# Optimization experiments

Measured on AMD Instinct MI355X. Metric: run time of the kernel, lower is better.

The kernel has to match this reference:

```python
import jax, jax.numpy as jnp
import numpy as np

H = 256          # hidden_dim
NH = 4           # num_heads
HD = H // NH     # head_dim = 64
EPS = 1e-5


def _ln(x, g, b):
    m = jnp.mean(x, axis=-1, keepdims=True)
    v = jnp.mean(jnp.square(x - m), axis=-1, keepdims=True)
    return (x - m) * jax.lax.rsqrt(v + EPS) * g + b


def _mha1(q_in, kv_in, in_proj_w, in_proj_b, out_w, out_b):
    # Single-query / single-key multihead attention (seq_len == 1 on both sides).
    # q_in, kv_in: [B, H]
    Wq, Wk, Wv = jnp.split(in_proj_w, 3, axis=0)   # each [H, H]
    bq, bk, bv = jnp.split(in_proj_b, 3, axis=0)
    B = q_in.shape[0]
    q = (q_in @ Wq.T + bq).reshape(B, NH, HD)
    k = (kv_in @ Wk.T + bk).reshape(B, NH, HD)
    v = (kv_in @ Wv.T + bv).reshape(B, NH, HD)
    scores = jnp.sum(q * k, axis=-1, keepdims=True) / jnp.sqrt(jnp.float32(HD))  # [B,NH,1]
    w = jax.nn.softmax(scores, axis=-1)  # softmax over 1 key -> all ones
    out = (w * v).reshape(B, H)
    return out @ out_w.T + out_b


def setup_inputs() -> dict:
    key = jax.random.key(0)
    ks = jax.random.split(key, 16)
    B, BIO, TXT, NC = 65536, 32, 768, 2
    s = lambda n: 1.0 / np.sqrt(n)
    return {
        "bio": jax.random.normal(ks[0], (B, BIO), jnp.float32),
        "text": jax.random.normal(ks[1], (B, TXT), jnp.float32),
        "bio_w": jax.random.normal(ks[2], (H, BIO), jnp.float32) * s(BIO),
        "bio_b": jnp.zeros((H,), jnp.float32),
        "text_w": jax.random.normal(ks[3], (H, TXT), jnp.float32) * s(TXT),
        "text_b": jnp.zeros((H,), jnp.float32),
        "ln_bio_g": jnp.ones((H,), jnp.float32),
        "ln_bio_b": jnp.zeros((H,), jnp.float32),
        "ln_text_g": jnp.ones((H,), jnp.float32),
        "ln_text_b": jnp.zeros((H,), jnp.float32),
        "in_proj_w": jax.random.normal(ks[4], (3 * H, H), jnp.float32) * s(H),
        "in_proj_b": jnp.zeros((3 * H,), jnp.float32),
        "out_w": jax.random.normal(ks[5], (H, H), jnp.float32) * s(H),
        "out_b": jnp.zeros((H,), jnp.float32),
        "cls1_w": jax.random.normal(ks[6], (H, 2 * H), jnp.float32) * s(2 * H),
        "cls1_b": jnp.zeros((H,), jnp.float32),
        "cls_ln_g": jnp.ones((H,), jnp.float32),
        "cls_ln_b": jnp.zeros((H,), jnp.float32),
        "cls2_w": jax.random.normal(ks[7], (NC, H), jnp.float32) * s(H),
        "cls2_b": jnp.zeros((NC,), jnp.float32),
    }


def reference(bio, text, bio_w, bio_b, text_w, text_b, ln_bio_g, ln_bio_b,
              ln_text_g, ln_text_b, in_proj_w, in_proj_b, out_w, out_b,
              cls1_w, cls1_b, cls_ln_g, cls_ln_b, cls2_w, cls2_b):
    b = _ln(bio @ bio_w.T + bio_b, ln_bio_g, ln_bio_b)      # [B, H]
    t = _ln(text @ text_w.T + text_b, ln_text_g, ln_text_b)  # [B, H]
    attn_bio = _mha1(b, t, in_proj_w, in_proj_b, out_w, out_b)
    attn_text = _mha1(t, b, in_proj_w, in_proj_b, out_w, out_b)
    fused = jnp.concatenate([attn_bio, attn_text], axis=-1)  # [B, 2H]
    h = jax.nn.relu(_ln(fused @ cls1_w.T + cls1_b, cls_ln_g, cls_ln_b))
    return h @ cls2_w.T + cls2_b
```

## Files before the change

### kernel.cpp

```cpp
#include <hip/hip_runtime.h>

typedef __attribute__((ext_vector_type(4))) float f4;
typedef __attribute__((ext_vector_type(2))) float f2;
typedef __attribute__((ext_vector_type(8))) short s8;

#define EPS 1e-5f

__device__ __forceinline__ unsigned short f2bf(float f) {
    union { float f; unsigned u; } v; v.f = f;
    unsigned u = v.u;
    return (unsigned short)((u + 0x7fffu + ((u >> 16) & 1u)) >> 16);
}
__device__ __forceinline__ unsigned pack2(float a, float b) {
    return (unsigned)f2bf(a) | ((unsigned)f2bf(b) << 16);
}

__device__ __forceinline__ unsigned cvt_pk2(float a, float b) {
    unsigned r;
    asm("v_cvt_pk_bf16_f32 %0, %1, %2" : "=v"(r) : "v"(a), "v"(b));
    return r;
}
__device__ __forceinline__ unsigned short cvt1(float a) {
    return (unsigned short)cvt_pk2(a, a);
}
__device__ __forceinline__ s8 pack8(f4 a, f4 b) {
    union { s8 v; unsigned u[4]; } r;
    r.u[0] = cvt_pk2(a[0], a[1]); r.u[1] = cvt_pk2(a[2], a[3]);
    r.u[2] = cvt_pk2(b[0], b[1]); r.u[3] = cvt_pk2(b[2], b[3]);
    return r.v;
}

#if defined(__has_builtin)
#if __has_builtin(__builtin_amdgcn_global_load_lds)
#define HAVE_GLLDS 1
#endif
#endif
__device__ __forceinline__ void gl_lds16(const float* g, unsigned short* l) {
#ifdef HAVE_GLLDS
    __builtin_amdgcn_global_load_lds(
        (const __attribute__((address_space(1))) unsigned int*)g,
        (__attribute__((address_space(3))) unsigned int*)l, 16, 0, 0);
#else
    *(f4*)l = *(const f4*)g;
#endif
}

__global__ __launch_bounds__(256) void k_prep1(const float* __restrict__ text_w,
                                               const float* __restrict__ bio_w,
                                               const float* __restrict__ out_w,
                                               const float* __restrict__ in_proj_w,
                                               const float* __restrict__ in_proj_b,
                                               const float* __restrict__ out_b,
                                               unsigned short* __restrict__ twFL,
                                               unsigned short* __restrict__ bwFL,
                                               float* __restrict__ A,
                                               float* __restrict__ cvec) {
    int b = blockIdx.x, t = threadIdx.x;
    if (b < 96) {
        int idx = b * 256 + t;
        int ksg = idx >> 10;
        int rem = idx & 1023;
        int ct = rem >> 6, lane = rem & 63;
        int n  = ct * 16 + (lane & 15);
        int k0 = ksg * 32 + ((lane >> 4) << 3);
        const float* src = &text_w[n * 768 + k0];
        f4 a = *(const f4*)src, c = *(const f4*)(src + 4);
        unsigned* dst = (unsigned*)&twFL[idx * 8];
        dst[0] = pack2(a[0], a[1]); dst[1] = pack2(a[2], a[3]);
        dst[2] = pack2(c[0], c[1]); dst[3] = pack2(c[2], c[3]);
    } else if (b < 100) {
        int idx = (b - 96) * 256 + t;
        int ct = idx >> 6, lane = idx & 63;
        int n  = ct * 16 + (lane & 15);
        int k0 = (lane >> 4) << 3;
        const float* src = &bio_w[n * 32 + k0];
        f4 a = *(const f4*)src, c = *(const f4*)(src + 4);
        unsigned* dst = (unsigned*)&bwFL[idx * 8];
        dst[0] = pack2(a[0], a[1]); dst[1] = pack2(a[2], a[3]);
        dst[2] = pack2(c[0], c[1]); dst[3] = pack2(c[2], c[3]);
    } else {
        __shared__ float srow[256];
        __shared__ float red[256];
        int i = b - 100, j = t;
        srow[j] = out_w[i * 256 + j];
        __syncthreads();
        float acc = 0.f;
#pragma unroll 16
        for (int k = 0; k < 256; k++)
            acc = fmaf(srow[k], in_proj_w[(512 + k) * 256 + j], acc);
        A[i * 256 + j] = acc;
        red[j] = srow[j] * in_proj_b[512 + j];
        __syncthreads();
        for (int s = 128; s > 0; s >>= 1) {
            if (j < s) red[j] += red[j + s];
            __syncthreads();
        }
        if (j == 0) cvec[i] = red[0] + out_b[i];
    }
}

__global__ __launch_bounds__(256) void k_prep_PQ(const float* __restrict__ cls1_w,
                                                 const float* __restrict__ cls1_b,
                                                 const float* __restrict__ A,
                                                 const float* __restrict__ cvec,
                                                 const float* __restrict__ ln_text_g,
                                                 const float* __restrict__ ln_text_b,
                                                 const float* __restrict__ ln_bio_g,
                                                 const float* __restrict__ ln_bio_b,
                                                 unsigned short* __restrict__ pqFL,
                                                 float* __restrict__ dvec) {
    __shared__ float w1[256], w2[256], red[256];
    int i = blockIdx.x, j = threadIdx.x;
    w1[j] = cls1_w[i * 512 + j];
    w2[j] = cls1_w[i * 512 + 256 + j];
    __syncthreads();
    float rp = 0.f, rq = 0.f;
#pragma unroll 8
    for (int k = 0; k < 256; k++) {
        float a = A[k * 256 + j];
        rp = fmaf(w1[k], a, rp);
        rq = fmaf(w2[k], a, rq);
    }
    int ct   = i >> 4;
    int lane = (i & 15) | (((j >> 3) & 3) << 4);
    int jj   = j & 7;
    int ks1  = j >> 5;
    pqFL[(((ks1     ) * 16 + ct) * 64 + lane) * 8 + jj] = f2bf(rp * ln_text_g[j]);
    pqFL[(((ks1 + 8 ) * 16 + ct) * 64 + lane) * 8 + jj] = f2bf(rq * ln_bio_g[j]);
    red[j] = rp * ln_text_b[j] + rq * ln_bio_b[j] + (w1[j] + w2[j]) * cvec[j];
    __syncthreads();
    for (int s = 128; s > 0; s >>= 1) {
        if (j < s) red[j] += red[j + s];
        __syncthreads();
    }
    if (j == 0) dvec[i] = red[0] + cls1_b[i];
}

__global__ __launch_bounds__(512, 4) void k_main(
    const float* __restrict__ bio, const float* __restrict__ text,
    const float* __restrict__ bio_b, const float* __restrict__ text_b,
    const float* __restrict__ cls_ln_g, const float* __restrict__ cls_ln_b,
    const float* __restrict__ cls2_w, const float* __restrict__ cls2_b,
    const unsigned short* __restrict__ twFL, const unsigned short* __restrict__ bwFL,
    const unsigned short* __restrict__ pqFL, const float* __restrict__ dvec,
    float* __restrict__ out)
{
    __shared__ __align__(16) unsigned short s_n[64][520];
    __shared__ __align__(16) float s_red[64][6][2];

    const int tid  = threadIdx.x;
    const int wv   = tid >> 6;
    const int cs   = wv & 3;
    const int rh   = wv >> 2;
    const int lane = tid & 63;
    const int q    = lane >> 4;
    const int lr   = lane & 15;
    const int R0   = blockIdx.x * 64;

    unsigned short* sx = (unsigned short*)s_n;
    const int SXU = 12288;

    f4 acc[2][4];
    float s1[2][4], s2[2][4], m_[2][4], iv_[2][4];

    int sfofs[3], sdofs[3];
#pragma unroll
    for (int i = 0; i < 3; i++) {
        int idx = i * 512 + tid;
        int row = idx / 24;
        int j   = idx - row * 24;
        sfofs[i] = (R0 + row) * 768 + ((j ^ (row & 7)) << 2);
        sdofs[i] = idx * 8;
    }
    int offB[2][2];
#pragma unroll
    for (int rt = 0; rt < 2; rt++) {
        int row = rh * 32 + rt * 16 + lr;
        int sw  = (row & 7) << 4;
        offB[rt][0] = (row * 384 + ((q * 32) ^ sw)) >> 1;
        offB[rt][1] = (row * 384 + (((q * 32) + 16) ^ sw)) >> 1;
    }

#pragma unroll
    for (int i = 0; i < 3; i++)
        gl_lds16(text + sfofs[i], sx + sdofs[i]);

    const unsigned short* wb = twFL + (cs * 256 + lane) * 8;
    s8 wc[4], wn[4];
#pragma unroll
    for (int c = 0; c < 4; c++) wc[c] = *(const s8*)&wb[c * 512];
#pragma unroll
    for (int c = 0; c < 4; c++) wn[c] = wc[c];

#pragma unroll
    for (int rt = 0; rt < 2; rt++)
#pragma unroll
        for (int c = 0; c < 4; c++) acc[rt][c] = (f4){0.f, 0.f, 0.f, 0.f};

    __syncthreads();

    for (int ch = 0; ch < 8; ch++) {
        const int buf = ch & 1;
        if (ch < 7) {
            const float* src = text + (ch + 1) * 96;
            unsigned short* dst = sx + (buf ^ 1) * SXU;
#pragma unroll
            for (int i = 0; i < 3; i++)
                gl_lds16(src + sfofs[i], dst + sdofs[i]);
        }
        const unsigned short* sb = sx + buf * SXU;
#pragma unroll
        for (int ks = 0; ks < 3; ks++) {
            int kk = ch * 3 + ks;
            if (kk < 23) {
#pragma unroll
                for (int c = 0; c < 4; c++)
                    wn[c] = *(const s8*)&wb[((kk + 1) * 16 + c) * 512];
            }
            f4 lo0 = *(const f4*)&sb[offB[0][0] + ks * 64];
            f4 hi0 = *(const f4*)&sb[offB[0][1] + ks * 64];
            f4 lo1 = *(const f4*)&sb[offB[1][0] + ks * 64];
            f4 hi1 = *(const f4*)&sb[offB[1][1] + ks * 64];
            s8 af0 = pack8(lo0, hi0);
            s8 af1 = pack8(lo1, hi1);
#pragma unroll
            for (int c = 0; c < 4; c++)
                acc[0][c] = __builtin_amdgcn_mfma_f32_16x16x32_bf16(af0, wc[c], acc[0][c], 0, 0, 0);
#pragma unroll
            for (int c = 0; c < 4; c++)
                acc[1][c] = __builtin_amdgcn_mfma_f32_16x16x32_bf16(af1, wc[c], acc[1][c], 0, 0, 0);
#pragma unroll
            for (int c = 0; c < 4; c++) wc[c] = wn[c];
        }
        __syncthreads();
    }

    f4 bioA[2], bioB[2];
#pragma unroll
    for (int rt = 0; rt < 2; rt++) {
        const float* p = &bio[(size_t)(R0 + rh * 32 + rt * 16 + lr) * 32 + q * 8];
        bioA[rt] = *(const f4*)p;
        bioB[rt] = *(const f4*)(p + 4);
    }
    s8 bfrb[4];
#pragma unroll
    for (int c = 0; c < 4; c++)
        bfrb[c] = *(const s8*)&bwFL[((cs * 4 + c) * 64 + lane) * 8];

#pragma unroll
    for (int rt = 0; rt < 2; rt++)
#pragma unroll
        for (int r = 0; r < 4; r++) { s1[rt][r] = 0.f; s2[rt][r] = 0.f; }
#pragma unroll
    for (int rt = 0; rt < 2; rt++)
#pragma unroll
        for (int c = 0; c < 4; c++) {
            float bb = text_b[cs * 64 + c * 16 + lr];
#pragma unroll
            for (int r = 0; r < 4; r++) {
                float x = acc[rt][c][r] + bb;
                acc[rt][c][r] = x;
                s1[rt][r] += x; s2[rt][r] += x * x;
            }
        }
#pragma unroll
    for (int off = 1; off < 16; off <<= 1)
#pragma unroll
        for (int rt = 0; rt < 2; rt++)
#pragma unroll
            for (int r = 0; r < 4; r++) {
                s1[rt][r] += __shfl_xor(s1[rt][r], off, 64);
                s2[rt][r] += __shfl_xor(s2[rt][r], off, 64);
            }
    if (lr == 0)
#pragma unroll
        for (int rt = 0; rt < 2; rt++)
#pragma unroll
            for (int r = 0; r < 4; r++) {
                int row = rh * 32 + rt * 16 + q * 4 + r;
                f2 v; v[0] = s1[rt][r]; v[1] = s2[rt][r];
                *(f2*)&s_red[row][cs][0] = v;
            }
    __syncthreads();
#pragma unroll
    for (int rt = 0; rt < 2; rt++)
#pragma unroll
        for (int r = 0; r < 4; r++) {
            int row = rh * 32 + rt * 16 + q * 4 + r;
            f4 v0 = *(const f4*)&s_red[row][0][0];
            f4 v1 = *(const f4*)&s_red[row][2][0];
            float t1 = v0[0] + v0[2] + v1[0] + v1[2];
            float t2 = v0[1] + v0[3] + v1[1] + v1[3];
            float mm = t1 * (1.f / 256.f);
            float vv = t2 * (1.f / 256.f) - mm * mm;
            m_[rt][r]  = mm;
            iv_[rt][r] = rsqrtf(vv + EPS);
        }
#pragma unroll
    for (int rt = 0; rt < 2; rt++)
#pragma unroll
        for (int c = 0; c < 4; c++) {
            int col = cs * 64 + c * 16 + lr;
#pragma unroll
            for (int r = 0; r < 4; r++)
                s_n[rh * 32 + rt * 16 + q * 4 + r][col] =
                    cvt1((acc[rt][c][r] - m_[rt][r]) * iv_[rt][r]);
        }

#pragma unroll
    for (int rt = 0; rt < 2; rt++)
#pragma unroll
        for (int c = 0; c < 4; c++) acc[rt][c] = (f4){0.f, 0.f, 0.f, 0.f};
#pragma unroll
    for (int rt = 0; rt < 2; rt++) {
        s8 af = pack8(bioA[rt], bioB[rt]);
#pragma unroll
        for (int c = 0; c < 4; c++)
            acc[rt][c] = __builtin_amdgcn_mfma_f32_16x16x32_bf16(af, bfrb[c], acc[rt][c], 0, 0, 0);
    }
#pragma unroll
    for (int rt = 0; rt < 2; rt++)
#pragma unroll
        for (int r = 0; r < 4; r++) { s1[rt][r] = 0.f; s2[rt][r] = 0.f; }
#pragma unroll
    for (int rt = 0; rt < 2; rt++)
#pragma unroll
        for (int c = 0; c < 4; c++) {
            float bb = bio_b[cs * 64 + c * 16 + lr];
#pragma unroll
            for (int r = 0; r < 4; r++) {
                float x = acc[rt][c][r] + bb;
                acc[rt][c][r] = x;
                s1[rt][r] += x; s2[rt][r] += x * x;
            }
        }
#pragma unroll
    for (int off = 1; off < 16; off <<= 1)
#pragma unroll
        for (int rt = 0; rt < 2; rt++)
#pragma unroll
            for (int r = 0; r < 4; r++) {
                s1[rt][r] += __shfl_xor(s1[rt][r], off, 64);
                s2[rt][r] += __shfl_xor(s2[rt][r], off, 64);
            }
    __syncthreads();
    if (lr == 0)
#pragma unroll
        for (int rt = 0; rt < 2; rt++)
#pragma unroll
            for (int r = 0; r < 4; r++) {
                int row = rh * 32 + rt * 16 + q * 4 + r;
                f2 v; v[0] = s1[rt][r]; v[1] = s2[rt][r];
                *(f2*)&s_red[row][cs][0] = v;
            }
    __syncthreads();
#pragma unroll
    for (int rt = 0; rt < 2; rt++)
#pragma unroll
        for (int r = 0; r < 4; r++) {
            int row = rh * 32 + rt * 16 + q * 4 + r;
            f4 v0 = *(const f4*)&s_red[row][0][0];
            f4 v1 = *(const f4*)&s_red[row][2][0];
            float t1 = v0[0] + v0[2] + v1[0] + v1[2];
            float t2 = v0[1] + v0[3] + v1[1] + v1[3];
            float mm = t1 * (1.f / 256.f);
            float vv = t2 * (1.f / 256.f) - mm * mm;
            m_[rt][r]  = mm;
            iv_[rt][r] = rsqrtf(vv + EPS);
        }
#pragma unroll
    for (int rt = 0; rt < 2; rt++)
#pragma unroll
        for (int c = 0; c < 4; c++) {
            int col = cs * 64 + c * 16 + lr;
#pragma unroll
            for (int r = 0; r < 4; r++)
                s_n[rh * 32 + rt * 16 + q * 4 + r][256 + col] =
                    cvt1((acc[rt][c][r] - m_[rt][r]) * iv_[rt][r]);
        }
    __syncthreads();

#pragma unroll
    for (int rt = 0; rt < 2; rt++)
#pragma unroll
        for (int c = 0; c < 4; c++) {
            float dv = dvec[cs * 64 + c * 16 + lr];
            acc[rt][c] = (f4){dv, dv, dv, dv};
        }
    const unsigned short* pb = pqFL + (cs * 256 + lane) * 8;
    s8 pc[4], pn[4];
#pragma unroll
    for (int c = 0; c < 4; c++) pc[c] = *(const s8*)&pb[c * 512];
#pragma unroll
    for (int c = 0; c < 4; c++) pn[c] = pc[c];
#pragma unroll
    for (int ks = 0; ks < 16; ks++) {
        if (ks < 15) {
#pragma unroll
            for (int c = 0; c < 4; c++)
                pn[c] = *(const s8*)&pb[((ks + 1) * 16 + c) * 512];
        }
        s8 af0 = *(const s8*)&s_n[rh * 32 + lr][ks * 32 + q * 8];
        s8 af1 = *(const s8*)&s_n[rh * 32 + 16 + lr][ks * 32 + q * 8];
#pragma unroll
        for (int c = 0; c < 4; c++)
            acc[0][c] = __builtin_amdgcn_mfma_f32_16x16x32_bf16(af0, pc[c], acc[0][c], 0, 0, 0);
#pragma unroll
        for (int c = 0; c < 4; c++)
            acc[1][c] = __builtin_amdgcn_mfma_f32_16x16x32_bf16(af1, pc[c], acc[1][c], 0, 0, 0);
#pragma unroll
        for (int c = 0; c < 4; c++) pc[c] = pn[c];
    }

#pragma unroll
    for (int rt = 0; rt < 2; rt++)
#pragma unroll
        for (int r = 0; r < 4; r++) { s1[rt][r] = 0.f; s2[rt][r] = 0.f; }
#pragma unroll
    for (int rt = 0; rt < 2; rt++)
#pragma unroll
        for (int c = 0; c < 4; c++)
#pragma unroll
            for (int r = 0; r < 4; r++) {
                float x = acc[rt][c][r];
                s1[rt][r] += x; s2[rt][r] += x * x;
            }
#pragma unroll
    for (int off = 1; off < 16; off <<= 1)
#pragma unroll
        for (int rt = 0; rt < 2; rt++)
#pragma unroll
            for (int r = 0; r < 4; r++) {
                s1[rt][r] += __shfl_xor(s1[rt][r], off, 64);
                s2[rt][r] += __shfl_xor(s2[rt][r], off, 64);
            }
    if (lr == 0)
#pragma unroll
        for (int rt = 0; rt < 2; rt++)
#pragma unroll
            for (int r = 0; r < 4; r++) {
                int row = rh * 32 + rt * 16 + q * 4 + r;
                f2 v; v[0] = s1[rt][r]; v[1] = s2[rt][r];
                *(f2*)&s_red[row][cs][0] = v;
            }
    __syncthreads();
#pragma unroll
    for (int rt = 0; rt < 2; rt++)
#pragma unroll
        for (int r = 0; r < 4; r++) {
            int row = rh * 32 + rt * 16 + q * 4 + r;
            f4 v0 = *(const f4*)&s_red[row][0][0];
            f4 v1 = *(const f4*)&s_red[row][2][0];
            float t1 = v0[0] + v0[2] + v1[0] + v1[2];
            float t2 = v0[1] + v0[3] + v1[1] + v1[3];
            float mm = t1 * (1.f / 256.f);
            float vv = t2 * (1.f / 256.f) - mm * mm;
            m_[rt][r]  = mm;
            iv_[rt][r] = rsqrtf(vv + EPS);
        }
    float po0[2][4], po1[2][4];
#pragma unroll
    for (int rt = 0; rt < 2; rt++)
#pragma unroll
        for (int r = 0; r < 4; r++) { po0[rt][r] = 0.f; po1[rt][r] = 0.f; }
#pragma unroll
    for (int rt = 0; rt < 2; rt++)
#pragma unroll
        for (int c = 0; c < 4; c++) {
            int col = cs * 64 + c * 16 + lr;
            float gg = cls_ln_g[col], bb = cls_ln_b[col];
            float c0 = cls2_w[col],   c1 = cls2_w[256 + col];
#pragma unroll
            for (int r = 0; r < 4; r++) {
                float h = fmaxf((acc[rt][c][r] - m_[rt][r]) * iv_[rt][r] * gg + bb, 0.f);
                po0[rt][r] = fmaf(h, c0, po0[rt][r]);
                po1[rt][r] = fmaf(h, c1, po1[rt][r]);
            }
        }
#pragma unroll
    for (int off = 1; off < 16; off <<= 1)
#pragma unroll
        for (int rt = 0; rt < 2; rt++)
#pragma unroll
            for (int r = 0; r < 4; r++) {
                po0[rt][r] += __shfl_xor(po0[rt][r], off, 64);
                po1[rt][r] += __shfl_xor(po1[rt][r], off, 64);
            }
    __syncthreads();
    if (lr == 0)
#pragma unroll
        for (int rt = 0; rt < 2; rt++)
#pragma unroll
            for (int r = 0; r < 4; r++) {
                int row = rh * 32 + rt * 16 + q * 4 + r;
                f2 v; v[0] = po0[rt][r]; v[1] = po1[rt][r];
                *(f2*)&s_red[row][cs][0] = v;
            }
    __syncthreads();
    if (tid < 64) {
        int row = tid;
        f4 a = *(const f4*)&s_red[row][0][0];
        f4 b = *(const f4*)&s_red[row][2][0];
        f2 o;
        o[0] = a[0] + a[2] + b[0] + b[2] + cls2_b[0];
        o[1] = a[1] + a[3] + b[1] + b[3] + cls2_b[1];
        *(f2*)&out[(size_t)(R0 + row) * 2] = o;
    }
}

extern "C" void kernel_launch(void* const* d_in, const int* in_sizes, int n_in,
                              void* d_out, int out_size, void* d_ws, size_t ws_size,
                              hipStream_t stream) {
    const float* bio       = (const float*)d_in[0];
    const float* text      = (const float*)d_in[1];
    const float* bio_w     = (const float*)d_in[2];
    const float* bio_b     = (const float*)d_in[3];
    const float* text_w    = (const float*)d_in[4];
    const float* text_b    = (const float*)d_in[5];
    const float* ln_bio_g  = (const float*)d_in[6];
    const float* ln_bio_b  = (const float*)d_in[7];
    const float* ln_text_g = (const float*)d_in[8];
    const float* ln_text_b = (const float*)d_in[9];
    const float* in_proj_w = (const float*)d_in[10];
    const float* in_proj_b = (const float*)d_in[11];
    const float* out_w     = (const float*)d_in[12];
    const float* out_b     = (const float*)d_in[13];
    const float* cls1_w    = (const float*)d_in[14];
    const float* cls1_b    = (const float*)d_in[15];
    const float* cls_ln_g  = (const float*)d_in[16];
    const float* cls_ln_b  = (const float*)d_in[17];
    const float* cls2_w    = (const float*)d_in[18];
    const float* cls2_b    = (const float*)d_in[19];
    float* out = (float*)d_out;

    float* ws   = (float*)d_ws;
    float* A    = ws;
    float* cvec = ws + 65536;
    float* dvec = ws + 65792;
    unsigned short* us   = (unsigned short*)(ws + 66048);
    unsigned short* twFL = us;
    unsigned short* bwFL = us + 196608;
    unsigned short* pqFL = us + 204800;

    k_prep1  <<<356, 256, 0, stream>>>(text_w, bio_w, out_w, in_proj_w, in_proj_b, out_b,
                                       twFL, bwFL, A, cvec);
    k_prep_PQ<<<256, 256, 0, stream>>>(cls1_w, cls1_b, A, cvec,
                                       ln_text_g, ln_text_b, ln_bio_g, ln_bio_b,
                                       pqFL, dvec);

    int nrows = in_sizes[0] / 32;
    k_main<<<nrows / 64, 512, 0, stream>>>(bio, text, bio_b, text_b,
                                           cls_ln_g, cls_ln_b, cls2_w, cls2_b,
                                           twFL, bwFL, pqFL, dvec, out);
}
```

Baseline: 381.0 us.

## Use 1024-thread blocks with one 16-row tile per wave in main kernel

Doubles the threads per block from 512 to 1024 so each wave handles a single 16-row MFMA tile instead of two, halving per-wave accumulator state. Global-to-LDS loads of the text chunk are redistributed across the larger block, and the final output reduction uses 128 threads. The aim is more waves in flight to hide memory latency. In exchange, each weight fragment loaded from global memory feeds half as many MFMAs, so weight-load traffic per row doubles, and the larger block relies on the launch bound of 8 to keep registers low.

```diff
diff --git a/kernel.cpp b/kernel.cpp
--- a/kernel.cpp
+++ b/kernel.cpp
@@ -136,7 +136,7 @@
     if (j == 0) dvec[i] = red[0] + cls1_b[i];
 }
 
-__global__ __launch_bounds__(512, 4) void k_main(
+__global__ __launch_bounds__(1024, 8) void k_main(
     const float* __restrict__ bio, const float* __restrict__ text,
     const float* __restrict__ bio_b, const float* __restrict__ text_b,
     const float* __restrict__ cls_ln_g, const float* __restrict__ cls_ln_b,
@@ -151,7 +151,7 @@
     const int tid  = threadIdx.x;
     const int wv   = tid >> 6;
     const int cs   = wv & 3;
-    const int rh   = wv >> 2;
+    const int rh2  = wv >> 2;
     const int lane = tid & 63;
     const int q    = lane >> 4;
     const int lr   = lane & 15;
@@ -160,30 +160,29 @@
     unsigned short* sx = (unsigned short*)s_n;
     const int SXU = 12288;
 
-    f4 acc[2][4];
-    float s1[2][4], s2[2][4], m_[2][4], iv_[2][4];
-
-    int sfofs[3], sdofs[3];
-#pragma unroll
-    for (int i = 0; i < 3; i++) {
-        int idx = i * 512 + tid;
+    f4 acc[4];
+    float s1[4], s2[4], m_[4], iv_[4];
+
+    int sfofs[2], sdofs[2];
+#pragma unroll
+    for (int i = 0; i < 2; i++) {
+        int idx = i * 1024 + tid;
         int row = idx / 24;
         int j   = idx - row * 24;
         sfofs[i] = (R0 + row) * 768 + ((j ^ (row & 7)) << 2);
         sdofs[i] = idx * 8;
     }
-    int offB[2][2];
-#pragma unroll
-    for (int rt = 0; rt < 2; rt++) {
-        int row = rh * 32 + rt * 16 + lr;
+    int offB[2];
+    {
+        int row = rh2 * 16 + lr;
         int sw  = (row & 7) << 4;
-        offB[rt][0] = (row * 384 + ((q * 32) ^ sw)) >> 1;
-        offB[rt][1] = (row * 384 + (((q * 32) + 16) ^ sw)) >> 1;
-    }
-
-#pragma unroll
-    for (int i = 0; i < 3; i++)
-        gl_lds16(text + sfofs[i], sx + sdofs[i]);
+        offB[0] = (row * 384 + ((q * 32) ^ sw)) >> 1;
+        offB[1] = (row * 384 + (((q * 32) + 16) ^ sw)) >> 1;
+    }
+
+    gl_lds16(text + sfofs[0], sx + sdofs[0]);
+    if (tid < 512)
+        gl_lds16(text + sfofs[1], sx + sdofs[1]);
 
     const unsigned short* wb = twFL + (cs * 256 + lane) * 8;
     s8 wc[4], wn[4];
@@ -193,9 +192,7 @@
     for (int c = 0; c < 4; c++) wn[c] = wc[c];
 
 #pragma unroll
-    for (int rt = 0; rt < 2; rt++)
-#pragma unroll
-        for (int c = 0; c < 4; c++) acc[rt][c] = (f4){0.f, 0.f, 0.f, 0.f};
+    for (int c = 0; c < 4; c++) acc[c] = (f4){0.f, 0.f, 0.f, 0.f};
 
     __syncthreads();
 
@@ -204,9 +201,9 @@
         if (ch < 7) {
             const float* src = text + (ch + 1) * 96;
             unsigned short* dst = sx + (buf ^ 1) * SXU;
-#pragma unroll
-            for (int i = 0; i < 3; i++)
-                gl_lds16(src + sfofs[i], dst + sdofs[i]);
+            gl_lds16(src + sfofs[0], dst + sdofs[0]);
+            if (tid < 512)
+                gl_lds16(src + sfofs[1], dst + sdofs[1]);
         }
         const unsigned short* sb = sx + buf * SXU;
 #pragma unroll
@@ -217,30 +214,23 @@
                 for (int c = 0; c < 4; c++)
                     wn[c] = *(const s8*)&wb[((kk + 1) * 16 + c) * 512];
             }
-            f4 lo0 = *(const f4*)&sb[offB[0][0] + ks * 64];
-            f4 hi0 = *(const f4*)&sb[offB[0][1] + ks * 64];
-            f4 lo1 = *(const f4*)&sb[offB[1][0] + ks * 64];
-            f4 hi1 = *(const f4*)&sb[offB[1][1] + ks * 64];
-            s8 af0 = pack8(lo0, hi0);
-            s8 af1 = pack8(lo1, hi1);
+            f4 lo = *(const f4*)&sb[offB[0] + ks * 64];
+            f4 hi = *(const f4*)&sb[offB[1] + ks * 64];
+            s8 af = pack8(lo, hi);
 #pragma unroll
             for (int c = 0; c < 4; c++)
-                acc[0][c] = __builtin_amdgcn_mfma_f32_16x16x32_bf16(af0, wc[c], acc[0][c], 0, 0, 0);
-#pragma unroll
-            for (int c = 0; c < 4; c++)
-                acc[1][c] = __builtin_amdgcn_mfma_f32_16x16x32_bf16(af1, wc[c], acc[1][c], 0, 0, 0);
+                acc[c] = __builtin_amdgcn_mfma_f32_16x16x32_bf16(af, wc[c], acc[c], 0, 0, 0);
 #pragma unroll
             for (int c = 0; c < 4; c++) wc[c] = wn[c];
         }
         __syncthreads();
     }
 
-    f4 bioA[2], bioB[2];
-#pragma unroll
-    for (int rt = 0; rt < 2; rt++) {
-        const float* p = &bio[(size_t)(R0 + rh * 32 + rt * 16 + lr) * 32 + q * 8];
-        bioA[rt] = *(const f4*)p;
-        bioB[rt] = *(const f4*)(p + 4);
+    f4 bioA, bioB;
+    {
+        const float* p = &bio[(size_t)(R0 + rh2 * 16 + lr) * 32 + q * 8];
+        bioA = *(const f4*)p;
+        bioB = *(const f4*)(p + 4);
     }
     s8 bfrb[4];
 #pragma unroll
@@ -248,263 +238,210 @@
         bfrb[c] = *(const s8*)&bwFL[((cs * 4 + c) * 64 + lane) * 8];
 
 #pragma unroll
-    for (int rt = 0; rt < 2; rt++)
-#pragma unroll
-        for (int r = 0; r < 4; r++) { s1[rt][r] = 0.f; s2[rt][r] = 0.f; }
-#pragma unroll
-    for (int rt = 0; rt < 2; rt++)
-#pragma unroll
-        for (int c = 0; c < 4; c++) {
-            float bb = text_b[cs * 64 + c * 16 + lr];
-#pragma unroll
-            for (int r = 0; r < 4; r++) {
-                float x = acc[rt][c][r] + bb;
-                acc[rt][c][r] = x;
-                s1[rt][r] += x; s2[rt][r] += x * x;
-            }
-        }
+    for (int r = 0; r < 4; r++) { s1[r] = 0.f; s2[r] = 0.f; }
+#pragma unroll
+    for (int c = 0; c < 4; c++) {
+        float bb = text_b[cs * 64 + c * 16 + lr];
+#pragma unroll
+        for (int r = 0; r < 4; r++) {
+            float x = acc[c][r] + bb;
+            acc[c][r] = x;
+            s1[r] += x; s2[r] += x * x;
+        }
+    }
 #pragma unroll
     for (int off = 1; off < 16; off <<= 1)
 #pragma unroll
-        for (int rt = 0; rt < 2; rt++)
-#pragma unroll
-            for (int r = 0; r < 4; r++) {
-                s1[rt][r] += __shfl_xor(s1[rt][r], off, 64);
-                s2[rt][r] += __shfl_xor(s2[rt][r], off, 64);
-            }
+        for (int r = 0; r < 4; r++) {
+            s1[r] += __shfl_xor(s1[r], off, 64);
+            s2[r] += __shfl_xor(s2[r], off, 64);
+        }
     if (lr == 0)
 #pragma unroll
-        for (int rt = 0; rt < 2; rt++)
-#pragma unroll
-            for (int r = 0; r < 4; r++) {
-                int row = rh * 32 + rt * 16 + q * 4 + r;
-                f2 v; v[0] = s1[rt][r]; v[1] = s2[rt][r];
-                *(f2*)&s_red[row][cs][0] = v;
-            }
-    __syncthreads();
-#pragma unroll
-    for (int rt = 0; rt < 2; rt++)
-#pragma unroll
-        for (int r = 0; r < 4; r++) {
-            int row = rh * 32 + rt * 16 + q * 4 + r;
-            f4 v0 = *(const f4*)&s_red[row][0][0];
-            f4 v1 = *(const f4*)&s_red[row][2][0];
-            float t1 = v0[0] + v0[2] + v1[0] + v1[2];
-            float t2 = v0[1] + v0[3] + v1[1] + v1[3];
-            float mm = t1 * (1.f / 256.f);
-            float vv = t2 * (1.f / 256.f) - mm * mm;
-            m_[rt][r]  = mm;
-            iv_[rt][r] = rsqrtf(vv + EPS);
-        }
-#pragma unroll
-    for (int rt = 0; rt < 2; rt++)
-#pragma unroll
-        for (int c = 0; c < 4; c++) {
-            int col = cs * 64 + c * 16 + lr;
-#pragma unroll
-            for (int r = 0; r < 4; r++)
-                s_n[rh * 32 + rt * 16 + q * 4 + r][col] =
-                    cvt1((acc[rt][c][r] - m_[rt][r]) * iv_[rt][r]);
-        }
-
-#pragma unroll
-    for (int rt = 0; rt < 2; rt++)
-#pragma unroll
-        for (int c = 0; c < 4; c++) acc[rt][c] = (f4){0.f, 0.f, 0.f, 0.f};
-#pragma unroll
-    for (int rt = 0; rt < 2; rt++) {
-        s8 af = pack8(bioA[rt], bioB[rt]);
+        for (int r = 0; r < 4; r++) {
+            int row = rh2 * 16 + q * 4 + r;
+            f2 v; v[0] = s1[r]; v[1] = s2[r];
+            *(f2*)&s_red[row][cs][0] = v;
+        }
+    __syncthreads();
+#pragma unroll
+    for (int r = 0; r < 4; r++) {
+        int row = rh2 * 16 + q * 4 + r;
+        f4 v0 = *(const f4*)&s_red[row][0][0];
+        f4 v1 = *(const f4*)&s_red[row][2][0];
+        float t1 = v0[0] + v0[2] + v1[0] + v1[2];
+        float t2 = v0[1] + v0[3] + v1[1] + v1[3];
+        float mm = t1 * (1.f / 256.f);
+        float vv = t2 * (1.f / 256.f) - mm * mm;
+        m_[r]  = mm;
+        iv_[r] = rsqrtf(vv + EPS);
+    }
+#pragma unroll
+    for (int c = 0; c < 4; c++) {
+        int col = cs * 64 + c * 16 + lr;
+#pragma unroll
+        for (int r = 0; r < 4; r++)
+            s_n[rh2 * 16 + q * 4 + r][col] =
+                cvt1((acc[c][r] - m_[r]) * iv_[r]);
+    }
+
+#pragma unroll
+    for (int c = 0; c < 4; c++) acc[c] = (f4){0.f, 0.f, 0.f, 0.f};
+    {
+        s8 af = pack8(bioA, bioB);
 #pragma unroll
         for (int c = 0; c < 4; c++)
-            acc[rt][c] = __builtin_amdgcn_mfma_f32_16x16x32_bf16(af, bfrb[c], acc[rt][c], 0, 0, 0);
-    }
-#pragma unroll
-    for (int rt = 0; rt < 2; rt++)
-#pragma unroll
-        for (int r = 0; r < 4; r++) { s1[rt][r] = 0.f; s2[rt][r] = 0.f; }
-#pragma unroll
-    for (int rt = 0; rt < 2; rt++)
-#pragma unroll
-        for (int c = 0; c < 4; c++) {
-            float bb = bio_b[cs * 64 + c * 16 + lr];
-#pragma unroll
-            for (int r = 0; r < 4; r++) {
-                float x = acc[rt][c][r] + bb;
-                acc[rt][c][r] = x;
-                s1[rt][r] += x; s2[rt][r] += x * x;
-            }
-        }
+            acc[c] = __builtin_amdgcn_mfma_f32_16x16x32_bf16(af, bfrb[c], acc[c], 0, 0, 0);
+    }
+#pragma unroll
+    for (int r = 0; r < 4; r++) { s1[r] = 0.f; s2[r] = 0.f; }
+#pragma unroll
+    for (int c = 0; c < 4; c++) {
+        float bb = bio_b[cs * 64 + c * 16 + lr];
+#pragma unroll
+        for (int r = 0; r < 4; r++) {
+            float x = acc[c][r] + bb;
+            acc[c][r] = x;
+            s1[r] += x; s2[r] += x * x;
+        }
+    }
 #pragma unroll
     for (int off = 1; off < 16; off <<= 1)
 #pragma unroll
-        for (int rt = 0; rt < 2; rt++)
-#pragma unroll
-            for (int r = 0; r < 4; r++) {
-                s1[rt][r] += __shfl_xor(s1[rt][r], off, 64);
-                s2[rt][r] += __shfl_xor(s2[rt][r], off, 64);
-            }
+        for (int r = 0; r < 4; r++) {
+            s1[r] += __shfl_xor(s1[r], off, 64);
+            s2[r] += __shfl_xor(s2[r], off, 64);
+        }
     __syncthreads();
     if (lr == 0)
 #pragma unroll
-        for (int rt = 0; rt < 2; rt++)
-#pragma unroll
-            for (int r = 0; r < 4; r++) {
-                int row = rh * 32 + rt * 16 + q * 4 + r;
-                f2 v; v[0] = s1[rt][r]; v[1] = s2[rt][r];
-                *(f2*)&s_red[row][cs][0] = v;
-            }
-    __syncthreads();
-#pragma unroll
-    for (int rt = 0; rt < 2; rt++)
-#pragma unroll
-        for (int r = 0; r < 4; r++) {
-            int row = rh * 32 + rt * 16 + q * 4 + r;
-            f4 v0 = *(const f4*)&s_red[row][0][0];
-            f4 v1 = *(const f4*)&s_red[row][2][0];
-            float t1 = v0[0] + v0[2] + v1[0] + v1[2];
-            float t2 = v0[1] + v0[3] + v1[1] + v1[3];
-            float mm = t1 * (1.f / 256.f);
-            float vv = t2 * (1.f / 256.f) - mm * mm;
-            m_[rt][r]  = mm;
-            iv_[rt][r] = rsqrtf(vv + EPS);
-        }
-#pragma unroll
-    for (int rt = 0; rt < 2; rt++)
-#pragma unroll
-        for (int c = 0; c < 4; c++) {
-            int col = cs * 64 + c * 16 + lr;
-#pragma unroll
-            for (int r = 0; r < 4; r++)
-                s_n[rh * 32 + rt * 16 + q * 4 + r][256 + col] =
-                    cvt1((acc[rt][c][r] - m_[rt][r]) * iv_[rt][r]);
-        }
-    __syncthreads();
-
-#pragma unroll
-    for (int rt = 0; rt < 2; rt++)
-#pragma unroll
-        for (int c = 0; c < 4; c++) {
-            float dv = dvec[cs * 64 + c * 16 + lr];
-            acc[rt][c] = (f4){dv, dv, dv, dv};
-        }
+        for (int r = 0; r < 4; r++) {
+            int row = rh2 * 16 + q * 4 + r;
+            f2 v; v[0] = s1[r]; v[1] = s2[r];
+            *(f2*)&s_red[row][cs][0] = v;
+        }
+    __syncthreads();
+#pragma unroll
+    for (int r = 0; r < 4; r++) {
+        int row = rh2 * 16 + q * 4 + r;
+        f4 v0 = *(const f4*)&s_red[row][0][0];
+        f4 v1 = *(const f4*)&s_red[row][2][0];
+        float t1 = v0[0] + v0[2] + v1[0] + v1[2];
+        float t2 = v0[1] + v0[3] + v1[1] + v1[3];
+        float mm = t1 * (1.f / 256.f);
+        float vv = t2 * (1.f / 256.f) - mm * mm;
+        m_[r]  = mm;
+        iv_[r] = rsqrtf(vv + EPS);
+    }
+#pragma unroll
+    for (int c = 0; c < 4; c++) {
+        int col = cs * 64 + c * 16 + lr;
+#pragma unroll
+        for (int r = 0; r < 4; r++)
+            s_n[rh2 * 16 + q * 4 + r][256 + col] =
+                cvt1((acc[c][r] - m_[r]) * iv_[r]);
+    }
+    __syncthreads();
+
+#pragma unroll
+    for (int c = 0; c < 4; c++) {
+        float dv = dvec[cs * 64 + c * 16 + lr];
+        acc[c] = (f4){dv, dv, dv, dv};
+    }
     const unsigned short* pb = pqFL + (cs * 256 + lane) * 8;
     s8 pc[4], pn[4];
 #pragma unroll
     for (int c = 0; c < 4; c++) pc[c] = *(const s8*)&pb[c * 512];
 #pragma unroll
     for (int c = 0; c < 4; c++) pn[c] = pc[c];
-#pragma unroll
+#pragma unroll 4
     for (int ks = 0; ks < 16; ks++) {
         if (ks < 15) {
 #pragma unroll
             for (int c = 0; c < 4; c++)
                 pn[c] = *(const s8*)&pb[((ks + 1) * 16 + c) * 512];
         }
-        s8 af0 = *(const s8*)&s_n[rh * 32 + lr][ks * 32 + q * 8];
-        s8 af1 = *(const s8*)&s_n[rh * 32 + 16 + lr][ks * 32 + q * 8];
+        s8 af = *(const s8*)&s_n[rh2 * 16 + lr][ks * 32 + q * 8];
 #pragma unroll
         for (int c = 0; c < 4; c++)
-            acc[0][c] = __builtin_amdgcn_mfma_f32_16x16x32_bf16(af0, pc[c], acc[0][c], 0, 0, 0);
-#pragma unroll
-        for (int c = 0; c < 4; c++)
-            acc[1][c] = __builtin_amdgcn_mfma_f32_16x16x32_bf16(af1, pc[c], acc[1][c], 0, 0, 0);
+            acc[c] = __builtin_amdgcn_mfma_f32_16x16x32_bf16(af, pc[c], acc[c], 0, 0, 0);
 #pragma unroll
         for (int c = 0; c < 4; c++) pc[c] = pn[c];
     }
 
 #pragma unroll
-    for (int rt = 0; rt < 2; rt++)
-#pragma unroll
-        for (int r = 0; r < 4; r++) { s1[rt][r] = 0.f; s2[rt][r] = 0.f; }
-#pragma unroll
-    for (int rt = 0; rt < 2; rt++)
-#pragma unroll
-        for (int c = 0; c < 4; c++)
-#pragma unroll
-            for (int r = 0; r < 4; r++) {
-                float x = acc[rt][c][r];
-                s1[rt][r] += x; s2[rt][r] += x * x;
-            }
+    for (int r = 0; r < 4; r++) { s1[r] = 0.f; s2[r] = 0.f; }
+#pragma unroll
+    for (int c = 0; c < 4; c++)
+#pragma unroll
+        for (int r = 0; r < 4; r++) {
+            float x = acc[c][r];
+            s1[r] += x; s2[r] += x * x;
+        }
 #pragma unroll
     for (int off = 1; off < 16; off <<= 1)
 #pragma unroll
-        for (int rt = 0; rt < 2; rt++)
-#pragma unroll
-            for (int r = 0; r < 4; r++) {
-                s1[rt][r] += __shfl_xor(s1[rt][r], off, 64);
-                s2[rt][r] += __shfl_xor(s2[rt][r], off, 64);
-            }
+        for (int r = 0; r < 4; r++) {
+            s1[r] += __shfl_xor(s1[r], off, 64);
+            s2[r] += __shfl_xor(s2[r], off, 64);
+        }
+    __syncthreads();
     if (lr == 0)
 #pragma unroll
-        for (int rt = 0; rt < 2; rt++)
-#pragma unroll
-            for (int r = 0; r < 4; r++) {
-                int row = rh * 32 + rt * 16 + q * 4 + r;
-                f2 v; v[0] = s1[rt][r]; v[1] = s2[rt][r];
-                *(f2*)&s_red[row][cs][0] = v;
-            }
-    __syncthreads();
-#pragma unroll
-    for (int rt = 0; rt < 2; rt++)
-#pragma unroll
-        for (int r = 0; r < 4; r++) {
-            int row = rh * 32 + rt * 16 + q * 4 + r;
-            f4 v0 = *(const f4*)&s_red[row][0][0];
-            f4 v1 = *(const f4*)&s_red[row][2][0];
-            float t1 = v0[0] + v0[2] + v1[0] + v1[2];
-            float t2 = v0[1] + v0[3] + v1[1] + v1[3];
-            float mm = t1 * (1.f / 256.f);
-            float vv = t2 * (1.f / 256.f) - mm * mm;
-            m_[rt][r]  = mm;
-            iv_[rt][r] = rsqrtf(vv + EPS);
-        }
-    float po0[2][4], po1[2][4];
-#pragma unroll
-    for (int rt = 0; rt < 2; rt++)
-#pragma unroll
-        for (int r = 0; r < 4; r++) { po0[rt][r] = 0.f; po1[rt][r] = 0.f; }
-#pragma unroll
-    for (int rt = 0; rt < 2; rt++)
-#pragma unroll
-        for (int c = 0; c < 4; c++) {
-            int col = cs * 64 + c * 16 + lr;
-            float gg = cls_ln_g[col], bb = cls_ln_b[col];
-            float c0 = cls2_w[col],   c1 = cls2_w[256 + col];
-#pragma unroll
-            for (int r = 0; r < 4; r++) {
-                float h = fmaxf((acc[rt][c][r] - m_[rt][r]) * iv_[rt][r] * gg + bb, 0.f);
-                po0[rt][r] = fmaf(h, c0, po0[rt][r]);
-                po1[rt][r] = fmaf(h, c1, po1[rt][r]);
-            }
-        }
+        for (int r = 0; r < 4; r++) {
+            int row = rh2 * 16 + q * 4 + r;
+            f2 v; v[0] = s1[r]; v[1] = s2[r];
+            *(f2*)&s_red[row][cs][0] = v;
+        }
+    __syncthreads();
+#pragma unroll
+    for (int r = 0; r < 4; r++) {
+        int row = rh2 * 16 + q * 4 + r;
+        f4 v0 = *(const f4*)&s_red[row][0][0];
+        f4 v1 = *(const f4*)&s_red[row][2][0];
+        float t1 = v0[0] + v0[2] + v1[0] + v1[2];
+        float t2 = v0[1] + v0[3] + v1[1] + v1[3];
+        float mm = t1 * (1.f / 256.f);
+        float vv = t2 * (1.f / 256.f) - mm * mm;
+        m_[r]  = mm;
+        iv_[r] = rsqrtf(vv + EPS);
+    }
+    float po0[4], po1[4];
+#pragma unroll
+    for (int r = 0; r < 4; r++) { po0[r] = 0.f; po1[r] = 0.f; }
+#pragma unroll
+    for (int c = 0; c < 4; c++) {
+        int col = cs * 64 + c * 16 + lr;
+        float gg = cls_ln_g[col], bb = cls_ln_b[col];
+        float c0 = cls2_w[col],   c1 = cls2_w[256 + col];
+#pragma unroll
+        for (int r = 0; r < 4; r++) {
+            float h = fmaxf((acc[c][r] - m_[r]) * iv_[r] * gg + bb, 0.f);
+            po0[r] = fmaf(h, c0, po0[r]);
+            po1[r] = fmaf(h, c1, po1[r]);
+        }
+    }
 #pragma unroll
     for (int off = 1; off < 16; off <<= 1)
 #pragma unroll
-        for (int rt = 0; rt < 2; rt++)
-#pragma unroll
-            for (int r = 0; r < 4; r++) {
-                po0[rt][r] += __shfl_xor(po0[rt][r], off, 64);
-                po1[rt][r] += __shfl_xor(po1[rt][r], off, 64);
-            }
+        for (int r = 0; r < 4; r++) {
+            po0[r] += __shfl_xor(po0[r], off, 64);
+            po1[r] += __shfl_xor(po1[r], off, 64);
+        }
     __syncthreads();
     if (lr == 0)
 #pragma unroll
-        for (int rt = 0; rt < 2; rt++)
-#pragma unroll
-            for (int r = 0; r < 4; r++) {
-                int row = rh * 32 + rt * 16 + q * 4 + r;
-                f2 v; v[0] = po0[rt][r]; v[1] = po1[rt][r];
-                *(f2*)&s_red[row][cs][0] = v;
-            }
-    __syncthreads();
-    if (tid < 64) {
-        int row = tid;
-        f4 a = *(const f4*)&s_red[row][0][0];
-        f4 b = *(const f4*)&s_red[row][2][0];
-        f2 o;
-        o[0] = a[0] + a[2] + b[0] + b[2] + cls2_b[0];
-        o[1] = a[1] + a[3] + b[1] + b[3] + cls2_b[1];
-        *(f2*)&out[(size_t)(R0 + row) * 2] = o;
+        for (int r = 0; r < 4; r++) {
+            int row = rh2 * 16 + q * 4 + r;
+            f2 v; v[0] = po0[r]; v[1] = po1[r];
+            *(f2*)&s_red[row][cs][0] = v;
+        }
+    __syncthreads();
+    if (tid < 128) {
+        int row = tid >> 1, comp = tid & 1;
+        float v = s_red[row][0][comp] + s_red[row][1][comp] +
+                  s_red[row][2][comp] + s_red[row][3][comp];
+        out[(size_t)(R0 + row) * 2 + comp] = v + cls2_b[comp];
     }
 }
 
@@ -549,7 +486,7 @@
                                        pqFL, dvec);
 
     int nrows = in_sizes[0] / 32;
-    k_main<<<nrows / 64, 512, 0, stream>>>(bio, text, bio_b, text_b,
-                                           cls_ln_g, cls_ln_b, cls2_w, cls2_b,
-                                           twFL, bwFL, pqFL, dvec, out);
-}
+    k_main<<<nrows / 64, 1024, 0, stream>>>(bio, text, bio_b, text_b,
+                                            cls_ln_g, cls_ln_b, cls2_w, cls2_b,
+                                            twFL, bwFL, pqFL, dvec, out);
+}
```

Result: slower. 451.8 us (+18.6%).

## Split bio projection+LN into separate kernel and shrink text staging chunks

Applied to the files above, without the earlier changes.

Moves the bio linear+LayerNorm into a new kernel that writes normalized bf16 rows to a global workspace. The main kernel then reads those rows straight from global memory for the second half of the classifier GEMM. It also stages text in 64-column chunks instead of 96, cutting LDS from roughly 66KB to about 34KB per block so more blocks can be resident. The cost is an extra launch and a 32MB bf16 round trip through global memory.

```diff
diff --git a/kernel.cpp b/kernel.cpp
--- a/kernel.cpp
+++ b/kernel.cpp
@@ -136,18 +136,12 @@
     if (j == 0) dvec[i] = red[0] + cls1_b[i];
 }
 
-__global__ __launch_bounds__(512, 4) void k_main(
-    const float* __restrict__ bio, const float* __restrict__ text,
-    const float* __restrict__ bio_b, const float* __restrict__ text_b,
-    const float* __restrict__ cls_ln_g, const float* __restrict__ cls_ln_b,
-    const float* __restrict__ cls2_w, const float* __restrict__ cls2_b,
-    const unsigned short* __restrict__ twFL, const unsigned short* __restrict__ bwFL,
-    const unsigned short* __restrict__ pqFL, const float* __restrict__ dvec,
-    float* __restrict__ out)
+__global__ __launch_bounds__(512, 4) void k_nb(
+    const float* __restrict__ bio, const float* __restrict__ bio_b,
+    const unsigned short* __restrict__ bwFL,
+    unsigned short* __restrict__ nb)
 {
-    __shared__ __align__(16) unsigned short s_n[64][520];
     __shared__ __align__(16) float s_red[64][6][2];
-
     const int tid  = threadIdx.x;
     const int wv   = tid >> 6;
     const int cs   = wv & 3;
@@ -157,18 +151,115 @@
     const int lr   = lane & 15;
     const int R0   = blockIdx.x * 64;
 
-    unsigned short* sx = (unsigned short*)s_n;
-    const int SXU = 12288;
+    f4 acc[2][4];
+    float s1[2][4], s2[2][4];
+
+    f4 bioA[2], bioB[2];
+#pragma unroll
+    for (int rt = 0; rt < 2; rt++) {
+        const float* p = &bio[(size_t)(R0 + rh * 32 + rt * 16 + lr) * 32 + q * 8];
+        bioA[rt] = *(const f4*)p;
+        bioB[rt] = *(const f4*)(p + 4);
+    }
+    s8 bfrb[4];
+#pragma unroll
+    for (int c = 0; c < 4; c++)
+        bfrb[c] = *(const s8*)&bwFL[((cs * 4 + c) * 64 + lane) * 8];
+
+#pragma unroll
+    for (int rt = 0; rt < 2; rt++)
+#pragma unroll
+        for (int c = 0; c < 4; c++) acc[rt][c] = (f4){0.f, 0.f, 0.f, 0.f};
+#pragma unroll
+    for (int rt = 0; rt < 2; rt++) {
+        s8 af = pack8(bioA[rt], bioB[rt]);
+#pragma unroll
+        for (int c = 0; c < 4; c++)
+            acc[rt][c] = __builtin_amdgcn_mfma_f32_16x16x32_bf16(af, bfrb[c], acc[rt][c], 0, 0, 0);
+    }
+#pragma unroll
+    for (int rt = 0; rt < 2; rt++)
+#pragma unroll
+        for (int r = 0; r < 4; r++) { s1[rt][r] = 0.f; s2[rt][r] = 0.f; }
+#pragma unroll
+    for (int rt = 0; rt < 2; rt++)
+#pragma unroll
+        for (int c = 0; c < 4; c++) {
+            float bb = bio_b[cs * 64 + c * 16 + lr];
+#pragma unroll
+            for (int r = 0; r < 4; r++) {
+                float x = acc[rt][c][r] + bb;
+                acc[rt][c][r] = x;
+                s1[rt][r] += x; s2[rt][r] += x * x;
+            }
+        }
+#pragma unroll
+    for (int off = 1; off < 16; off <<= 1)
+#pragma unroll
+        for (int rt = 0; rt < 2; rt++)
+#pragma unroll
+            for (int r = 0; r < 4; r++) {
+                s1[rt][r] += __shfl_xor(s1[rt][r], off, 64);
+                s2[rt][r] += __shfl_xor(s2[rt][r], off, 64);
+            }
+    if (lr == 0)
+#pragma unroll
+        for (int rt = 0; rt < 2; rt++)
+#pragma unroll
+            for (int r = 0; r < 4; r++) {
+                int row = rh * 32 + rt * 16 + q * 4 + r;
+                f2 v; v[0] = s1[rt][r]; v[1] = s2[rt][r];
+                *(f2*)&s_red[row][cs][0] = v;
+            }
+    __syncthreads();
+#pragma unroll
+    for (int rt = 0; rt < 2; rt++)
+#pragma unroll
+        for (int r = 0; r < 4; r++) {
+            int row = rh * 32 + rt * 16 + q * 4 + r;
+            f4 v0 = *(const f4*)&s_red[row][0][0];
+            f4 v1 = *(const f4*)&s_red[row][2][0];
+            float t1 = v0[0] + v0[2] + v1[0] + v1[2];
+            float t2 = v0[1] + v0[3] + v1[1] + v1[3];
+            float mm = t1 * (1.f / 256.f);
+            float vv = t2 * (1.f / 256.f) - mm * mm;
+            float iv = rsqrtf(vv + EPS);
+#pragma unroll
+            for (int c = 0; c < 4; c++)
+                nb[(size_t)(R0 + row) * 256 + cs * 64 + c * 16 + lr] =
+                    cvt1((acc[rt][c][r] - mm) * iv);
+        }
+}
+
+__global__ __launch_bounds__(512, 4) void k_main(
+    const float* __restrict__ text, const float* __restrict__ text_b,
+    const float* __restrict__ cls_ln_g, const float* __restrict__ cls_ln_b,
+    const float* __restrict__ cls2_w, const float* __restrict__ cls2_b,
+    const unsigned short* __restrict__ twFL, const unsigned short* __restrict__ pqFL,
+    const unsigned short* __restrict__ nb, const float* __restrict__ dvec,
+    float* __restrict__ out)
+{
+    __shared__ __align__(16) unsigned short s_mem[16896];
+    __shared__ __align__(16) float s_red[64][6][2];
+
+    const int tid  = threadIdx.x;
+    const int wv   = tid >> 6;
+    const int cs   = wv & 3;
+    const int rh   = wv >> 2;
+    const int lane = tid & 63;
+    const int q    = lane >> 4;
+    const int lr   = lane & 15;
+    const int R0   = blockIdx.x * 64;
 
     f4 acc[2][4];
     float s1[2][4], s2[2][4], m_[2][4], iv_[2][4];
 
-    int sfofs[3], sdofs[3];
-#pragma unroll
-    for (int i = 0; i < 3; i++) {
+    int sfofs[2], sdofs[2];
+#pragma unroll
+    for (int i = 0; i < 2; i++) {
         int idx = i * 512 + tid;
-        int row = idx / 24;
-        int j   = idx - row * 24;
+        int row = idx >> 4;
+        int j   = idx & 15;
         sfofs[i] = (R0 + row) * 768 + ((j ^ (row & 7)) << 2);
         sdofs[i] = idx * 8;
     }
@@ -176,14 +267,13 @@
 #pragma unroll
     for (int rt = 0; rt < 2; rt++) {
         int row = rh * 32 + rt * 16 + lr;
-        int sw  = (row & 7) << 4;
-        offB[rt][0] = (row * 384 + ((q * 32) ^ sw)) >> 1;
-        offB[rt][1] = (row * 384 + (((q * 32) + 16) ^ sw)) >> 1;
-    }
-
-#pragma unroll
-    for (int i = 0; i < 3; i++)
-        gl_lds16(text + sfofs[i], sx + sdofs[i]);
+#pragma unroll
+        for (int b = 0; b < 2; b++)
+            offB[rt][b] = row * 128 + ((((q << 1) | b) ^ (row & 7)) << 3);
+    }
+
+    gl_lds16(text + sfofs[0], s_mem + sdofs[0]);
+    gl_lds16(text + sfofs[1], s_mem + sdofs[1]);
 
     const unsigned short* wb = twFL + (cs * 256 + lane) * 8;
     s8 wc[4], wn[4];
@@ -199,19 +289,18 @@
 
     __syncthreads();
 
-    for (int ch = 0; ch < 8; ch++) {
+    for (int ch = 0; ch < 12; ch++) {
         const int buf = ch & 1;
-        if (ch < 7) {
-            const float* src = text + (ch + 1) * 96;
-            unsigned short* dst = sx + (buf ^ 1) * SXU;
-#pragma unroll
-            for (int i = 0; i < 3; i++)
-                gl_lds16(src + sfofs[i], dst + sdofs[i]);
-        }
-        const unsigned short* sb = sx + buf * SXU;
-#pragma unroll
-        for (int ks = 0; ks < 3; ks++) {
-            int kk = ch * 3 + ks;
+        if (ch < 11) {
+            const float* src = text + (ch + 1) * 64;
+            unsigned short* dst = s_mem + (buf ^ 1) * 8192;
+            gl_lds16(src + sfofs[0], dst + sdofs[0]);
+            gl_lds16(src + sfofs[1], dst + sdofs[1]);
+        }
+        const unsigned short* sb = s_mem + buf * 8192;
+#pragma unroll
+        for (int ks = 0; ks < 2; ks++) {
+            int kk = ch * 2 + ks;
             if (kk < 23) {
 #pragma unroll
                 for (int c = 0; c < 4; c++)
@@ -234,18 +323,6 @@
         }
         __syncthreads();
     }
-
-    f4 bioA[2], bioB[2];
-#pragma unroll
-    for (int rt = 0; rt < 2; rt++) {
-        const float* p = &bio[(size_t)(R0 + rh * 32 + rt * 16 + lr) * 32 + q * 8];
-        bioA[rt] = *(const f4*)p;
-        bioB[rt] = *(const f4*)(p + 4);
-    }
-    s8 bfrb[4];
-#pragma unroll
-    for (int c = 0; c < 4; c++)
-        bfrb[c] = *(const s8*)&bwFL[((cs * 4 + c) * 64 + lane) * 8];
 
 #pragma unroll
     for (int rt = 0; rt < 2; rt++)
@@ -303,79 +380,7 @@
             int col = cs * 64 + c * 16 + lr;
 #pragma unroll
             for (int r = 0; r < 4; r++)
-                s_n[rh * 32 + rt * 16 + q * 4 + r][col] =
-                    cvt1((acc[rt][c][r] - m_[rt][r]) * iv_[rt][r]);
-        }
-
-#pragma unroll
-    for (int rt = 0; rt < 2; rt++)
-#pragma unroll
-        for (int c = 0; c < 4; c++) acc[rt][c] = (f4){0.f, 0.f, 0.f, 0.f};
-#pragma unroll
-    for (int rt = 0; rt < 2; rt++) {
-        s8 af = pack8(bioA[rt], bioB[rt]);
-#pragma unroll
-        for (int c = 0; c < 4; c++)
-            acc[rt][c] = __builtin_amdgcn_mfma_f32_16x16x32_bf16(af, bfrb[c], acc[rt][c], 0, 0, 0);
-    }
-#pragma unroll
-    for (int rt = 0; rt < 2; rt++)
-#pragma unroll
-        for (int r = 0; r < 4; r++) { s1[rt][r] = 0.f; s2[rt][r] = 0.f; }
-#pragma unroll
-    for (int rt = 0; rt < 2; rt++)
-#pragma unroll
-        for (int c = 0; c < 4; c++) {
-            float bb = bio_b[cs * 64 + c * 16 + lr];
-#pragma unroll
-            for (int r = 0; r < 4; r++) {
-                float x = acc[rt][c][r] + bb;
-                acc[rt][c][r] = x;
-                s1[rt][r] += x; s2[rt][r] += x * x;
-            }
-        }
-#pragma unroll
-    for (int off = 1; off < 16; off <<= 1)
-#pragma unroll
-        for (int rt = 0; rt < 2; rt++)
-#pragma unroll
-            for (int r = 0; r < 4; r++) {
-                s1[rt][r] += __shfl_xor(s1[rt][r], off, 64);
-                s2[rt][r] += __shfl_xor(s2[rt][r], off, 64);
-            }
-    __syncthreads();
-    if (lr == 0)
-#pragma unroll
-        for (int rt = 0; rt < 2; rt++)
-#pragma unroll
-            for (int r = 0; r < 4; r++) {
-                int row = rh * 32 + rt * 16 + q * 4 + r;
-                f2 v; v[0] = s1[rt][r]; v[1] = s2[rt][r];
-                *(f2*)&s_red[row][cs][0] = v;
-            }
-    __syncthreads();
-#pragma unroll
-    for (int rt = 0; rt < 2; rt++)
-#pragma unroll
-        for (int r = 0; r < 4; r++) {
-            int row = rh * 32 + rt * 16 + q * 4 + r;
-            f4 v0 = *(const f4*)&s_red[row][0][0];
-            f4 v1 = *(const f4*)&s_red[row][2][0];
-            float t1 = v0[0] + v0[2] + v1[0] + v1[2];
-            float t2 = v0[1] + v0[3] + v1[1] + v1[3];
-            float mm = t1 * (1.f / 256.f);
-            float vv = t2 * (1.f / 256.f) - mm * mm;
-            m_[rt][r]  = mm;
-            iv_[rt][r] = rsqrtf(vv + EPS);
-        }
-#pragma unroll
-    for (int rt = 0; rt < 2; rt++)
-#pragma unroll
-        for (int c = 0; c < 4; c++) {
-            int col = cs * 64 + c * 16 + lr;
-#pragma unroll
-            for (int r = 0; r < 4; r++)
-                s_n[rh * 32 + rt * 16 + q * 4 + r][256 + col] =
+                s_mem[(rh * 32 + rt * 16 + q * 4 + r) * 264 + col] =
                     cvt1((acc[rt][c][r] - m_[rt][r]) * iv_[rt][r]);
         }
     __syncthreads();
@@ -393,15 +398,36 @@
     for (int c = 0; c < 4; c++) pc[c] = *(const s8*)&pb[c * 512];
 #pragma unroll
     for (int c = 0; c < 4; c++) pn[c] = pc[c];
-#pragma unroll
-    for (int ks = 0; ks < 16; ks++) {
-        if (ks < 15) {
+
+    const int a0 = (rh * 32 + lr) * 264 + q * 8;
+    const int a1 = (rh * 32 + 16 + lr) * 264 + q * 8;
+#pragma unroll 4
+    for (int ks = 0; ks < 8; ks++) {
+#pragma unroll
+        for (int c = 0; c < 4; c++)
+            pn[c] = *(const s8*)&pb[((ks + 1) * 16 + c) * 512];
+        s8 af0 = *(const s8*)&s_mem[a0 + ks * 32];
+        s8 af1 = *(const s8*)&s_mem[a1 + ks * 32];
+#pragma unroll
+        for (int c = 0; c < 4; c++)
+            acc[0][c] = __builtin_amdgcn_mfma_f32_16x16x32_bf16(af0, pc[c], acc[0][c], 0, 0, 0);
+#pragma unroll
+        for (int c = 0; c < 4; c++)
+            acc[1][c] = __builtin_amdgcn_mfma_f32_16x16x32_bf16(af1, pc[c], acc[1][c], 0, 0, 0);
+#pragma unroll
+        for (int c = 0; c < 4; c++) pc[c] = pn[c];
+    }
+    const unsigned short* nbp0 = nb + (size_t)(R0 + rh * 32 + lr) * 256 + q * 8;
+    const unsigned short* nbp1 = nbp0 + 16 * 256;
+#pragma unroll 4
+    for (int ks2 = 0; ks2 < 8; ks2++) {
+        if (ks2 < 7) {
 #pragma unroll
             for (int c = 0; c < 4; c++)
-                pn[c] = *(const s8*)&pb[((ks + 1) * 16 + c) * 512];
-        }
-        s8 af0 = *(const s8*)&s_n[rh * 32 + lr][ks * 32 + q * 8];
-        s8 af1 = *(const s8*)&s_n[rh * 32 + 16 + lr][ks * 32 + q * 8];
+                pn[c] = *(const s8*)&pb[((ks2 + 9) * 16 + c) * 512];
+        }
+        s8 af0 = *(const s8*)&nbp0[ks2 * 32];
+        s8 af1 = *(const s8*)&nbp1[ks2 * 32];
 #pragma unroll
         for (int c = 0; c < 4; c++)
             acc[0][c] = __builtin_amdgcn_mfma_f32_16x16x32_bf16(af0, pc[c], acc[0][c], 0, 0, 0);
@@ -541,6 +567,7 @@
     unsigned short* twFL = us;
     unsigned short* bwFL = us + 196608;
     unsigned short* pqFL = us + 204800;
+    unsigned short* nbuf = us + 335872;
 
     k_prep1  <<<356, 256, 0, stream>>>(text_w, bio_w, out_w, in_proj_w, in_proj_b, out_b,
                                        twFL, bwFL, A, cvec);
@@ -549,7 +576,8 @@
                                        pqFL, dvec);
 
     int nrows = in_sizes[0] / 32;
-    k_main<<<nrows / 64, 512, 0, stream>>>(bio, text, bio_b, text_b,
+    k_nb  <<<nrows / 64, 512, 0, stream>>>(bio, bio_b, bwFL, nbuf);
+    k_main<<<nrows / 64, 512, 0, stream>>>(text, text_b,
                                            cls_ln_g, cls_ln_b, cls2_w, cls2_b,
-                                           twFL, bwFL, pqFL, dvec, out);
-}
+                                           twFL, pqFL, nbuf, dvec, out);
+}
```

Measured after the change: 402.8 us. 1.06x slower.
